# Kernel tuning notes

Hardware: AMD Instinct MI355X
Metric: run time of the kernel (lower is better)

## Reference

```python
import jax, jax.numpy as jnp
import numpy as np

D_MODEL = 2048
K_DIM = 128
V_DIM = 128
H = 16
B = 1
S = 2048
SCALE_BASE = 512.0
THETA = 10000.0
EPS = 1e-5


def setup_inputs() -> dict:
    key = jax.random.key(0)
    ks = jax.random.split(key, 11)
    lin = lambda k, i, o: jax.random.normal(k, (i, o), jnp.float32) * 0.02
    return {
        "x": jax.random.normal(ks[0], (B, S, D_MODEL), jnp.float32),
        "Wq": lin(ks[1], D_MODEL, K_DIM * H), "bq": jnp.zeros((K_DIM * H,), jnp.float32),
        "Wk": lin(ks[2], D_MODEL, K_DIM * H), "bk": jnp.zeros((K_DIM * H,), jnp.float32),
        "Wv": lin(ks[3], D_MODEL, V_DIM * H), "bv": jnp.zeros((V_DIM * H,), jnp.float32),
        "Wg": lin(ks[4], D_MODEL, V_DIM * H), "bg": jnp.zeros((V_DIM * H,), jnp.float32),
        "Wo": lin(ks[5], V_DIM * H, D_MODEL), "bo": jnp.zeros((D_MODEL,), jnp.float32),
    }


def _rotate_half(x):
    # interleaved pairs: (x0, x1, x2, x3, ...) -> (-x1, x0, -x3, x2, ...)
    xr = x.reshape(*x.shape[:-1], -1, 2)
    x1, x2 = xr[..., 0], xr[..., 1]
    return jnp.stack((-x2, x1), axis=-1).reshape(x.shape)


def _rope_xpos(q, k, seq_len, dim):
    pos = jnp.arange(seq_len, dtype=jnp.float32)
    inv_freq = 1.0 / (THETA ** (jnp.arange(0, dim, 2, dtype=jnp.float32) / dim))
    freqs = jnp.repeat(pos[:, None] * inv_freq[None, :], 2, axis=-1)  # (S, dim)
    cos, sin = jnp.cos(freqs), jnp.sin(freqs)
    sbase = (jnp.arange(0, dim, 2, dtype=jnp.float32) + 0.4 * dim) / (1.4 * dim)
    power = (pos - seq_len // 2) / SCALE_BASE
    scale = jnp.repeat(sbase[None, :] ** power[:, None], 2, axis=-1)  # (S, dim)
    q = (q * cos + _rotate_half(q) * sin) * scale
    k = (k * cos + _rotate_half(k) * sin) / scale
    return q, k


def reference(x, Wq, bq, Wk, bk, Wv, bv, Wg, bg, Wo, bo):
    Bb, Ss, Dd = x.shape
    heads = lambda t: t.reshape(Bb, Ss, H, -1).transpose(0, 2, 1, 3)  # (B,H,S,d)
    q = heads(x @ Wq + bq)
    k = heads(x @ Wk + bk)
    v = heads(x @ Wv + bv)
    q, k = _rope_xpos(q, k, Ss, K_DIM)
    # per-head decay gamma_h = 1 - 2^{-5-h}
    gamma = 1.0 - 2.0 ** (-5.0 - jnp.arange(H, dtype=jnp.float32))
    pos = jnp.arange(Ss, dtype=jnp.float32)
    pm = pos[:, None] - pos[None, :]  # (S,S)
    decay_mask = jnp.where(pm >= 0, gamma[:, None, None] ** jnp.maximum(pm, 0.0), 0.0)  # (H,S,S)
    scores = jnp.einsum('bhid,bhjd->bhij', q, k) * decay_mask
    ret = jnp.einsum('bhij,bhjd->bhid', scores, v)  # (B,H,S,V_DIM)
    # concat heads and GroupNorm (num_groups=H, affine=False) over flattened rows
    concat = ret.transpose(0, 2, 1, 3).reshape(Bb * Ss, H, V_DIM)
    mu = concat.mean(-1, keepdims=True)
    var = ((concat - mu) ** 2).mean(-1, keepdims=True)
    gn = ((concat - mu) / jnp.sqrt(var + EPS)).reshape(Bb, Ss, H * V_DIM)
    out = (jax.nn.silu(x @ Wg + bg) * gn) @ Wo + bo
    return out
```

## Files before the change

kernel.cpp:

```cpp
#include <hip/hip_runtime.h>
#include <hip/hip_bf16.h>

#define S 2048
#define DM 2048
#define H 16
#define HD 128

using bf16 = __hip_bfloat16;
typedef __attribute__((ext_vector_type(8))) short bf16x8;
typedef __attribute__((ext_vector_type(8))) unsigned short u16x8;
typedef __attribute__((ext_vector_type(4))) float f32x4;

__device__ __forceinline__ unsigned short f2bu(float f) {
  bf16 b = __float2bfloat16(f);
  union { bf16 b; unsigned short u; } cv; cv.b = b; return cv.u;
}
__device__ __forceinline__ float bu2f(unsigned short u) {
  union { bf16 b; unsigned short u; } cv; cv.u = u; return __bfloat162float(cv.b);
}

__device__ __forceinline__ void async_copy16(const void* g, void* l) {
  __builtin_amdgcn_global_load_lds(
      (const __attribute__((address_space(1))) void*)g,
      (__attribute__((address_space(3))) void*)l, 16, 0, 0);
}

__global__ __launch_bounds__(256) void cvt_kernel(const float* __restrict__ x,
                                                  unsigned short* __restrict__ o) {
  int i = (blockIdx.x * 256 + threadIdx.x) * 4;
  float4 v = *(const float4*)(x + i);
  ushort4 r;
  r.x = f2bu(v.x); r.y = f2bu(v.y); r.z = f2bu(v.z); r.w = f2bu(v.w);
  *(ushort4*)(o + i) = r;
}

__global__ __launch_bounds__(256) void wtrans_kernel(
    const float* __restrict__ s0, const float* __restrict__ s1, const float* __restrict__ s2,
    const float* __restrict__ s3, const float* __restrict__ s4,
    unsigned short* __restrict__ d0, unsigned short* __restrict__ d1, unsigned short* __restrict__ d2,
    unsigned short* __restrict__ d3, unsigned short* __restrict__ d4) {
  __shared__ float tile[64][65];
  int z = blockIdx.z;
  const float* src = z == 0 ? s0 : z == 1 ? s1 : z == 2 ? s2 : z == 3 ? s3 : s4;
  unsigned short* dst = z == 0 ? d0 : z == 1 ? d1 : z == 2 ? d2 : z == 3 ? d3 : d4;
  int tid = threadIdx.x;
  int by = blockIdx.y * 64;
  int bx = blockIdx.x * 64;
  int r0 = tid >> 4;
  int c0 = (tid & 15) * 4;
#pragma unroll
  for (int i = 0; i < 4; i++) {
    int row = r0 + i * 16;
    float4 t = *(const float4*)(src + (size_t)(by + row) * DM + bx + c0);
    tile[row][c0 + 0] = t.x; tile[row][c0 + 1] = t.y;
    tile[row][c0 + 2] = t.z; tile[row][c0 + 3] = t.w;
  }
  __syncthreads();
#pragma unroll
  for (int i = 0; i < 4; i++) {
    int nrow = r0 + i * 16;
    ushort4 o;
    o.x = f2bu(tile[c0 + 0][nrow]);
    o.y = f2bu(tile[c0 + 1][nrow]);
    o.z = f2bu(tile[c0 + 2][nrow]);
    o.w = f2bu(tile[c0 + 3][nrow]);
    *(ushort4*)(dst + (size_t)(bx + nrow) * DM + by + c0) = o;
  }
}

__global__ __launch_bounds__(256) void vtrans_kernel(const unsigned short* __restrict__ v,
                                                     unsigned short* __restrict__ vt) {
  __shared__ unsigned short tile[64][72];
  int tid = threadIdx.x;
  int by = blockIdx.y * 64, bx = blockIdx.x * 64;
  int r0 = tid >> 3;
  int c0 = (tid & 7) * 8;
#pragma unroll
  for (int i = 0; i < 2; i++) {
    int row = r0 + i * 32;
    u16x8 t = *(const u16x8*)(v + (size_t)(by + row) * DM + bx + c0);
#pragma unroll
    for (int j = 0; j < 8; j++) tile[row][c0 + j] = t[j];
  }
  __syncthreads();
#pragma unroll
  for (int i = 0; i < 2; i++) {
    int nrow = r0 + i * 32;
    u16x8 o;
#pragma unroll
    for (int j = 0; j < 8; j++) o[j] = tile[c0 + j][nrow];
    *(u16x8*)(vt + (size_t)(bx + nrow) * DM + by + c0) = o;
  }
}

__device__ __forceinline__ void stage_half(const unsigned short* gbase, char* ldsbase, int tid) {
#pragma unroll
  for (int r = 0; r < 2; r++) {
    int a = r * 8192 + tid * 16;
    int row = a >> 7;
    int cb = (a & 127) ^ ((row & 7) << 4);
    async_copy16((const unsigned char*)(gbase + (size_t)row * DM) + cb, ldsbase + a);
  }
}

__global__ __launch_bounds__(512, 2) void gemm_qkvg_kernel(
    const unsigned short* __restrict__ A, const unsigned short* __restrict__ Bm,
    const float* __restrict__ bias0, const float* __restrict__ bias1,
    const float* __restrict__ bias2, const float* __restrict__ bias3,
    unsigned short* __restrict__ C0, unsigned short* __restrict__ C1,
    unsigned short* __restrict__ C2, unsigned short* __restrict__ C3) {
  __shared__ alignas(16) char smem[131072];
  char* sA = smem;
  char* sB = smem + 65536;
  int tid = threadIdx.x;
  int wg = blockIdx.y * 32 + blockIdx.x;
  int xcd = wg & 7, rr0 = wg >> 3;
  int bm = (rr0 >> 2) * 256;
  int bn = (xcd * 4 + (rr0 & 3)) * 256;
  int wid = tid >> 6, lane = tid & 63;
  int wm = wid >> 2, wn = wid & 3;
  int r16 = lane & 15, quad = lane >> 4;
  f32x4 acc[8][4] = {};
  bf16x8 bfrag[2][4];
  const int bhalf = (wn >> 1) << 14;
  const int blr0 = ((wn & 1) << 6) + r16;

  stage_half(Bm + (size_t)bn * DM, sB, tid);
  stage_half(Bm + (size_t)(bn + 128) * DM, sB + 16384, tid);
  stage_half(A + (size_t)bm * DM, sA, tid);
  stage_half(A + (size_t)(bm + 128) * DM, sA + 16384, tid);
  asm volatile("s_waitcnt vmcnt(0)" ::: "memory");
  __builtin_amdgcn_s_barrier();

  for (int t = 0; t < 32; ++t) {
    const int buf = (t & 1) << 15;
    const int nbuf = buf ^ 32768;
    const bool more = t < 31;
    const int kn = (t + 1) * 64;
    char* sAc = sA + buf;
    char* sBc = sB + buf;
    bf16x8 afrag[4];

#pragma unroll
    for (int nt = 0; nt < 4; ++nt) {
      int lr = blr0 + nt * 16;
      bfrag[0][nt] = *(const bf16x8*)(sBc + bhalf + lr * 128 + ((quad * 16) ^ ((lr & 7) << 4)));
    }
#pragma unroll
    for (int mt = 0; mt < 4; ++mt) {
      int lr = mt * 32 + wm * 16 + r16;
      afrag[mt] = *(const bf16x8*)(sAc + lr * 128 + ((quad * 16) ^ ((lr & 7) << 4)));
    }
    if (more) {
      stage_half(Bm + (size_t)bn * DM + kn, sB + nbuf, tid);
      stage_half(Bm + (size_t)(bn + 128) * DM + kn, sB + nbuf + 16384, tid);
      stage_half(A + (size_t)bm * DM + kn, sA + nbuf, tid);
    }
    __builtin_amdgcn_s_barrier();
    asm volatile("s_waitcnt lgkmcnt(0)" ::: "memory");
    __builtin_amdgcn_s_setprio(1);
#pragma unroll
    for (int mt = 0; mt < 4; ++mt)
#pragma unroll
      for (int nt = 0; nt < 4; ++nt)
        acc[mt][nt] = __builtin_amdgcn_mfma_f32_16x16x32_bf16(afrag[mt], bfrag[0][nt], acc[mt][nt], 0, 0, 0);
    __builtin_amdgcn_s_setprio(0);
    __builtin_amdgcn_s_barrier();

#pragma unroll
    for (int nt = 0; nt < 4; ++nt) {
      int lr = blr0 + nt * 16;
      bfrag[1][nt] = *(const bf16x8*)(sBc + bhalf + lr * 128 + ((64 + quad * 16) ^ ((lr & 7) << 4)));
    }
#pragma unroll
    for (int mt = 0; mt < 4; ++mt) {
      int lr = mt * 32 + wm * 16 + r16;
      afrag[mt] = *(const bf16x8*)(sAc + lr * 128 + ((64 + quad * 16) ^ ((lr & 7) << 4)));
    }
    __builtin_amdgcn_s_barrier();
    asm volatile("s_waitcnt lgkmcnt(0)" ::: "memory");
    __builtin_amdgcn_s_setprio(1);
#pragma unroll
    for (int mt = 0; mt < 4; ++mt)
#pragma unroll
      for (int nt = 0; nt < 4; ++nt)
        acc[mt][nt] = __builtin_amdgcn_mfma_f32_16x16x32_bf16(afrag[mt], bfrag[1][nt], acc[mt][nt], 0, 0, 0);
    __builtin_amdgcn_s_setprio(0);
    if (more) { asm volatile("s_waitcnt vmcnt(6)" ::: "memory"); }
    else      { asm volatile("s_waitcnt vmcnt(0)" ::: "memory"); }
    __builtin_amdgcn_s_barrier();

#pragma unroll
    for (int mt = 0; mt < 4; ++mt) {
      int lr = mt * 32 + wm * 16 + r16;
      afrag[mt] = *(const bf16x8*)(sAc + 16384 + lr * 128 + ((quad * 16) ^ ((lr & 7) << 4)));
    }
    if (more) stage_half(A + (size_t)(bm + 128) * DM + kn, sA + nbuf + 16384, tid);
    __builtin_amdgcn_s_barrier();
    asm volatile("s_waitcnt lgkmcnt(0)" ::: "memory");
    __builtin_amdgcn_s_setprio(1);
#pragma unroll
    for (int mt = 0; mt < 4; ++mt)
#pragma unroll
      for (int nt = 0; nt < 4; ++nt)
        acc[4 + mt][nt] = __builtin_amdgcn_mfma_f32_16x16x32_bf16(afrag[mt], bfrag[0][nt], acc[4 + mt][nt], 0, 0, 0);
    __builtin_amdgcn_s_setprio(0);
    __builtin_amdgcn_s_barrier();

#pragma unroll
    for (int mt = 0; mt < 4; ++mt) {
      int lr = mt * 32 + wm * 16 + r16;
      afrag[mt] = *(const bf16x8*)(sAc + 16384 + lr * 128 + ((64 + quad * 16) ^ ((lr & 7) << 4)));
    }
    __builtin_amdgcn_s_barrier();
    asm volatile("s_waitcnt lgkmcnt(0)" ::: "memory");
    __builtin_amdgcn_s_setprio(1);
#pragma unroll
    for (int mt = 0; mt < 4; ++mt)
#pragma unroll
      for (int nt = 0; nt < 4; ++nt)
        acc[4 + mt][nt] = __builtin_amdgcn_mfma_f32_16x16x32_bf16(afrag[mt], bfrag[1][nt], acc[4 + mt][nt], 0, 0, 0);
    __builtin_amdgcn_s_setprio(0);
    if (more) { asm volatile("s_waitcnt vmcnt(2)" ::: "memory"); }
    __builtin_amdgcn_s_barrier();
  }

  int ch = bn >> 11;
  const float* bp = ch == 0 ? bias0 : ch == 1 ? bias1 : ch == 2 ? bias2 : bias3;
  unsigned short* Cp = ch == 0 ? C0 : ch == 1 ? C1 : ch == 2 ? C2 : C3;
  int lcb = bn & 2047;
#pragma unroll
  for (int nt = 0; nt < 4; ++nt) {
    int lc = lcb + wn * 64 + nt * 16 + r16;
    float bv = bp[lc];
#pragma unroll
    for (int mt = 0; mt < 8; ++mt) {
      int m0 = bm + (mt >> 2) * 128 + (mt & 3) * 32 + wm * 16 + quad * 4;
#pragma unroll
      for (int rrr = 0; rrr < 4; ++rrr)
        Cp[(size_t)(m0 + rrr) * DM + lc] = f2bu(acc[mt][nt][rrr] + bv);
    }
  }
}

__global__ __launch_bounds__(256) void gemm_out_kernel(
    const unsigned short* __restrict__ A, const unsigned short* __restrict__ Bp,
    const float* __restrict__ bias, float* __restrict__ C) {
  __shared__ alignas(16) unsigned char sA[16384];
  __shared__ alignas(16) unsigned char sB[16384];
  int tid = threadIdx.x;
  int bm = blockIdx.y * 128, bn = blockIdx.x * 128;
  int wid = tid >> 6, lane = tid & 63;
  int wm = wid >> 1, wn = wid & 1;
  int r16 = lane & 15, quad = lane >> 4;
  f32x4 acc[4][4] = {};
  for (int kt = 0; kt < DM; kt += 64) {
#pragma unroll
    for (int r = 0; r < 4; r++) {
      int a = r * 4096 + tid * 16;
      int row = a >> 7;
      int cb = (a & 127) ^ ((row & 7) << 4);
      async_copy16((const unsigned char*)(A + (size_t)(bm + row) * DM + kt) + cb, sA + a);
      async_copy16((const unsigned char*)(Bp + (size_t)(bn + row) * DM + kt) + cb, sB + a);
    }
    __syncthreads();
#pragma unroll
    for (int kk = 0; kk < 2; kk++) {
      bf16x8 af[4], bfr[4];
#pragma unroll
      for (int mt = 0; mt < 4; mt++) {
        int row = wm * 64 + mt * 16 + r16;
        af[mt] = *(const bf16x8*)(sA + row * 128 + ((quad * 16 + kk * 64) ^ ((row & 7) << 4)));
      }
#pragma unroll
      for (int nt = 0; nt < 4; nt++) {
        int row = wn * 64 + nt * 16 + r16;
        bfr[nt] = *(const bf16x8*)(sB + row * 128 + ((quad * 16 + kk * 64) ^ ((row & 7) << 4)));
      }
#pragma unroll
      for (int mt = 0; mt < 4; mt++)
#pragma unroll
        for (int nt = 0; nt < 4; nt++)
          acc[mt][nt] = __builtin_amdgcn_mfma_f32_16x16x32_bf16(af[mt], bfr[nt], acc[mt][nt], 0, 0, 0);
    }
    __syncthreads();
  }
#pragma unroll
  for (int nt = 0; nt < 4; nt++) {
    int n = bn + wn * 64 + nt * 16 + r16;
    float bv = bias[n];
#pragma unroll
    for (int mt = 0; mt < 4; mt++) {
      int m0 = bm + wm * 64 + mt * 16 + quad * 4;
#pragma unroll
      for (int r = 0; r < 4; r++)
        C[(size_t)(m0 + r) * DM + n] = acc[mt][nt][r] + bv;
    }
  }
}

__global__ __launch_bounds__(256) void rope_kernel(unsigned short* __restrict__ q,
                                                   unsigned short* __restrict__ k) {
  int idx = blockIdx.x * 256 + threadIdx.x;
  int s = idx >> 10;
  int p = idx & 1023;
  int t = p & 63;
  int head = p >> 6;
  int col = (head << 7) + (t << 1);
  size_t off = (size_t)s * DM + col;
  float ang = (float)s * exp2f((float)(-2 * t) * (13.287712379549449f / 128.0f));
  float sn, cs;
  sincosf(ang, &sn, &cs);
  float sb = ((float)(2 * t) + 51.2f) * (1.0f / 179.2f);
  float power = ((float)s - 1024.0f) * (1.0f / 512.0f);
  float scale = exp2f(power * log2f(sb));
  float l2g = log2f(1.0f - exp2f((float)(-5 - head)));
  float qsc = scale * exp2f((float)s * l2g);
  float ksc = (1.0f / scale) * exp2f(-(float)s * l2g);
  unsigned int qu = *(unsigned int*)(q + off);
  float a = bu2f(qu & 0xffff), b = bu2f(qu >> 16);
  float qa = (a * cs - b * sn) * qsc;
  float qb2 = (b * cs + a * sn) * qsc;
  *(unsigned int*)(q + off) = (unsigned int)f2bu(qa) | ((unsigned int)f2bu(qb2) << 16);
  unsigned int ku = *(unsigned int*)(k + off);
  float c2 = bu2f(ku & 0xffff), d2 = bu2f(ku >> 16);
  float ka = (c2 * cs - d2 * sn) * ksc;
  float kb2 = (d2 * cs + c2 * sn) * ksc;
  *(unsigned int*)(k + off) = (unsigned int)f2bu(ka) | ((unsigned int)f2bu(kb2) << 16);
}

__device__ __forceinline__ void stage_kv(const unsigned short* __restrict__ k,
                                         const unsigned short* __restrict__ vt,
                                         int h, int J0, unsigned char* dK,
                                         unsigned char* dV, int tid) {
#pragma unroll
  for (int r = 0; r < 4; r++) {
    int a = r * 4096 + tid * 16;
    int rowk = a >> 8;
    int cbk = (a & 255) ^ ((rowk & 7) << 4);
    async_copy16((const unsigned char*)(k + (size_t)(J0 + rowk) * DM + h * HD) + cbk, dK + a);
    int rowv = a >> 7;
    int cbv = (a & 127) ^ ((rowv & 7) << 4);
    async_copy16((const unsigned char*)(vt + (size_t)(h * HD + rowv) * DM + J0) + cbv, dV + a);
  }
}

__global__ __launch_bounds__(256) void retention_kernel(
    const unsigned short* __restrict__ q, const unsigned short* __restrict__ k,
    const unsigned short* __restrict__ vt, float* __restrict__ ret) {
  __shared__ alignas(16) unsigned char sK[2][16384];
  __shared__ alignas(16) unsigned char sV[2][16384];
  __shared__ alignas(16) unsigned char Plds[8192];
  int bx = blockIdx.x;
  int hi = bx >> 8;
  int h = ((bx >> 5) & 7) | (hi << 3);
  int ib = hi ? (bx & 31) : (31 - (bx & 31));
  int I = ib << 6;
  int tid = threadIdx.x, wid = tid >> 6, lane = tid & 63;
  int r16 = lane & 15, quad = lane >> 4;
  bf16x8 aQ[4];
  size_t qrow = (size_t)(I + wid * 16 + r16);
#pragma unroll
  for (int kk = 0; kk < 4; kk++)
    aQ[kk] = *(const bf16x8*)(q + qrow * DM + h * HD + kk * 32 + quad * 8);
  f32x4 acc[8] = {};
  unsigned char* Pw = Plds + wid * 2048;
  stage_kv(k, vt, h, 0, sK[0], sV[0], tid);
  for (int J0 = 0; J0 <= I; J0 += 64) {
    int cur = (J0 >> 6) & 1;
    bool more = (J0 + 64) <= I;
    if (more) stage_kv(k, vt, h, J0 + 64, sK[cur ^ 1], sV[cur ^ 1], tid);
    if (more) { asm volatile("s_waitcnt vmcnt(8)" ::: "memory"); }
    else      { asm volatile("s_waitcnt vmcnt(0)" ::: "memory"); }
    __builtin_amdgcn_s_barrier();
    const unsigned char* sKc = sK[cur];
    const unsigned char* sVc = sV[cur];
    f32x4 sf[4] = {};
#pragma unroll
    for (int nt = 0; nt < 4; nt++) {
      int row = nt * 16 + r16;
#pragma unroll
      for (int kk = 0; kk < 4; kk++) {
        bf16x8 bK = *(const bf16x8*)(sKc + row * 256 + ((kk * 64 + quad * 16) ^ ((row & 7) << 4)));
        sf[nt] = __builtin_amdgcn_mfma_f32_16x16x32_bf16(aQ[kk], bK, sf[nt], 0, 0, 0);
      }
    }
    bool diag = (J0 == I);
#pragma unroll
    for (int nt = 0; nt < 4; nt++) {
      int j = nt * 16 + r16;
#pragma unroll
      for (int r = 0; r < 4; r++) {
        int ii = wid * 16 + quad * 4 + r;
        float pv = sf[nt][r];
        if (diag && (ii - j) < 0) pv = 0.0f;
        int pr = quad * 4 + r;
        int pcb = (nt * 16 + r16) * 2;
        *(unsigned short*)(Pw + pr * 128 + (pcb ^ ((pr & 7) << 4))) = f2bu(pv);
      }
    }
#pragma unroll
    for (int kk2 = 0; kk2 < 2; kk2++) {
      int cb = kk2 * 64 + quad * 16;
      bf16x8 aP = *(const bf16x8*)(Pw + r16 * 128 + (cb ^ ((r16 & 7) << 4)));
#pragma unroll
      for (int nt2 = 0; nt2 < 8; nt2++) {
        int row = nt2 * 16 + r16;
        bf16x8 bV = *(const bf16x8*)(sVc + row * 128 + ((kk2 * 64 + quad * 16) ^ ((row & 7) << 4)));
        acc[nt2] = __builtin_amdgcn_mfma_f32_16x16x32_bf16(aP, bV, acc[nt2], 0, 0, 0);
      }
    }
    __builtin_amdgcn_s_barrier();
  }
#pragma unroll
  for (int nt2 = 0; nt2 < 8; nt2++) {
    int dcol = h * HD + nt2 * 16 + r16;
#pragma unroll
    for (int r = 0; r < 4; r++) {
      int i = I + wid * 16 + quad * 4 + r;
      ret[(size_t)i * DM + dcol] = acc[nt2][r];
    }
  }
}

__global__ __launch_bounds__(256) void gn_gate_kernel(const float* __restrict__ ret,
                                                      const unsigned short* __restrict__ g,
                                                      unsigned short* __restrict__ y) {
  int tid = threadIdx.x;
  int wave = tid >> 6, lane = tid & 63;
  int gidx = blockIdx.x * 4 + wave;
  int s = gidx >> 4, h = gidx & 15;
  size_t base = (size_t)s * DM + h * HD + lane * 2;
  float2 v = *(const float2*)(ret + base);
  float sum = v.x + v.y;
  float sq = v.x * v.x + v.y * v.y;
#pragma unroll
  for (int o = 32; o > 0; o >>= 1) {
    sum += __shfl_xor(sum, o, 64);
    sq += __shfl_xor(sq, o, 64);
  }
  float mean = sum * 0.0078125f;
  float var = sq * 0.0078125f - mean * mean;
  float rstd = rsqrtf(var + 1e-5f);
  unsigned int gu = *(const unsigned int*)(g + base);
  float g0 = bu2f(gu & 0xffff), g1 = bu2f(gu >> 16);
  float s0 = g0 / (1.0f + expf(-g0));
  float s1 = g1 / (1.0f + expf(-g1));
  float y0 = s0 * (v.x - mean) * rstd;
  float y1 = s1 * (v.y - mean) * rstd;
  *(unsigned int*)(y + base) = (unsigned int)f2bu(y0) | ((unsigned int)f2bu(y1) << 16);
}

extern "C" void kernel_launch(void* const* d_in, const int* in_sizes, int n_in,
                              void* d_out, int out_size, void* d_ws, size_t ws_size,
                              hipStream_t stream) {
  (void)in_sizes; (void)n_in; (void)out_size; (void)ws_size;
  const float* x  = (const float*)d_in[0];
  const float* Wq = (const float*)d_in[1];
  const float* bq = (const float*)d_in[2];
  const float* Wk = (const float*)d_in[3];
  const float* bk = (const float*)d_in[4];
  const float* Wv = (const float*)d_in[5];
  const float* bv = (const float*)d_in[6];
  const float* Wg = (const float*)d_in[7];
  const float* bg = (const float*)d_in[8];
  const float* Wo = (const float*)d_in[9];
  const float* bo = (const float*)d_in[10];

  char* ws = (char*)d_ws;
  const size_t MB = 1ull << 20;
  unsigned short* xb   = (unsigned short*)(ws + 0 * MB);
  unsigned short* wcat = (unsigned short*)(ws + 8 * MB);
  unsigned short* wto  = (unsigned short*)(ws + 40 * MB);
  unsigned short* qb   = (unsigned short*)(ws + 48 * MB);
  unsigned short* kb   = (unsigned short*)(ws + 56 * MB);
  unsigned short* vb   = (unsigned short*)(ws + 64 * MB);
  unsigned short* gb   = (unsigned short*)(ws + 72 * MB);
  unsigned short* vt   = (unsigned short*)(ws + 80 * MB);
  float*          rt   = (float*)(ws + 88 * MB);
  unsigned short* yb   = (unsigned short*)(ws + 104 * MB);

  cvt_kernel<<<4096, 256, 0, stream>>>(x, xb);
  wtrans_kernel<<<dim3(32, 32, 5), 256, 0, stream>>>(
      Wq, Wk, Wv, Wg, Wo,
      wcat, wcat + (size_t)2048 * DM, wcat + (size_t)4096 * DM, wcat + (size_t)6144 * DM, wto);
  gemm_qkvg_kernel<<<dim3(32, 8), 512, 0, stream>>>(
      xb, wcat, bq, bk, bv, bg, qb, kb, vb, gb);
  rope_kernel<<<8192, 256, 0, stream>>>(qb, kb);
  vtrans_kernel<<<dim3(32, 32), 256, 0, stream>>>(vb, vt);
  retention_kernel<<<512, 256, 0, stream>>>(qb, kb, vt, rt);
  gn_gate_kernel<<<8192, 256, 0, stream>>>(rt, gb, yb);
  gemm_out_kernel<<<dim3(16, 16), 256, 0, stream>>>(yb, wto, bo, (float*)d_out);
}
```

Baseline: 191.6 us.

## Fuse V transpose into QKVG GEMM epilogue and GroupNorm+gate into retention

The QKVG GEMM now writes the V slice directly in transposed layout, which removes the separate vtrans kernel. The retention kernel computes the per-head GroupNorm statistics and the SiLU gate in registers and writes bf16 y. This drops the fp32 ret round trip and the gn_gate launch. The GEMM also changes its workgroup-to-tile swizzle and spreads its async prefetch stages across the four MFMA phases, with the vmcnt waits adjusted to match. The trade-offs are strided transposed stores in the V epilogue and scalar 2-byte gate loads and y stores in the retention epilogue.

```diff
diff --git a/kernel.cpp b/kernel.cpp
--- a/kernel.cpp
+++ b/kernel.cpp
@@ -68,31 +68,6 @@
   }
 }
 
-__global__ __launch_bounds__(256) void vtrans_kernel(const unsigned short* __restrict__ v,
-                                                     unsigned short* __restrict__ vt) {
-  __shared__ unsigned short tile[64][72];
-  int tid = threadIdx.x;
-  int by = blockIdx.y * 64, bx = blockIdx.x * 64;
-  int r0 = tid >> 3;
-  int c0 = (tid & 7) * 8;
-#pragma unroll
-  for (int i = 0; i < 2; i++) {
-    int row = r0 + i * 32;
-    u16x8 t = *(const u16x8*)(v + (size_t)(by + row) * DM + bx + c0);
-#pragma unroll
-    for (int j = 0; j < 8; j++) tile[row][c0 + j] = t[j];
-  }
-  __syncthreads();
-#pragma unroll
-  for (int i = 0; i < 2; i++) {
-    int nrow = r0 + i * 32;
-    u16x8 o;
-#pragma unroll
-    for (int j = 0; j < 8; j++) o[j] = tile[c0 + j][nrow];
-    *(u16x8*)(vt + (size_t)(bx + nrow) * DM + by + c0) = o;
-  }
-}
-
 __device__ __forceinline__ void stage_half(const unsigned short* gbase, char* ldsbase, int tid) {
 #pragma unroll
   for (int r = 0; r < 2; r++) {
@@ -108,15 +83,15 @@
     const float* __restrict__ bias0, const float* __restrict__ bias1,
     const float* __restrict__ bias2, const float* __restrict__ bias3,
     unsigned short* __restrict__ C0, unsigned short* __restrict__ C1,
-    unsigned short* __restrict__ C2, unsigned short* __restrict__ C3) {
+    unsigned short* __restrict__ Vt, unsigned short* __restrict__ C3) {
   __shared__ alignas(16) char smem[131072];
   char* sA = smem;
   char* sB = smem + 65536;
   int tid = threadIdx.x;
   int wg = blockIdx.y * 32 + blockIdx.x;
-  int xcd = wg & 7, rr0 = wg >> 3;
-  int bm = (rr0 >> 2) * 256;
-  int bn = (xcd * 4 + (rr0 & 3)) * 256;
+  int swz = (wg & 7) * 32 + (wg >> 3);
+  int bm = (swz >> 5) * 256;
+  int bn = (swz & 31) * 256;
   int wid = tid >> 6, lane = tid & 63;
   int wm = wid >> 2, wn = wid & 3;
   int r16 = lane & 15, quad = lane >> 4;
@@ -151,11 +126,7 @@
       int lr = mt * 32 + wm * 16 + r16;
       afrag[mt] = *(const bf16x8*)(sAc + lr * 128 + ((quad * 16) ^ ((lr & 7) << 4)));
     }
-    if (more) {
-      stage_half(Bm + (size_t)bn * DM + kn, sB + nbuf, tid);
-      stage_half(Bm + (size_t)(bn + 128) * DM + kn, sB + nbuf + 16384, tid);
-      stage_half(A + (size_t)bm * DM + kn, sA + nbuf, tid);
-    }
+    if (more) stage_half(Bm + (size_t)bn * DM + kn, sB + nbuf, tid);
     __builtin_amdgcn_s_barrier();
     asm volatile("s_waitcnt lgkmcnt(0)" ::: "memory");
     __builtin_amdgcn_s_setprio(1);
@@ -177,6 +148,7 @@
       int lr = mt * 32 + wm * 16 + r16;
       afrag[mt] = *(const bf16x8*)(sAc + lr * 128 + ((64 + quad * 16) ^ ((lr & 7) << 4)));
     }
+    if (more) stage_half(Bm + (size_t)(bn + 128) * DM + kn, sB + nbuf + 16384, tid);
     __builtin_amdgcn_s_barrier();
     asm volatile("s_waitcnt lgkmcnt(0)" ::: "memory");
     __builtin_amdgcn_s_setprio(1);
@@ -186,7 +158,7 @@
       for (int nt = 0; nt < 4; ++nt)
         acc[mt][nt] = __builtin_amdgcn_mfma_f32_16x16x32_bf16(afrag[mt], bfrag[1][nt], acc[mt][nt], 0, 0, 0);
     __builtin_amdgcn_s_setprio(0);
-    if (more) { asm volatile("s_waitcnt vmcnt(6)" ::: "memory"); }
+    if (more) { asm volatile("s_waitcnt vmcnt(4)" ::: "memory"); }
     else      { asm volatile("s_waitcnt vmcnt(0)" ::: "memory"); }
     __builtin_amdgcn_s_barrier();
 
@@ -195,7 +167,7 @@
       int lr = mt * 32 + wm * 16 + r16;
       afrag[mt] = *(const bf16x8*)(sAc + 16384 + lr * 128 + ((quad * 16) ^ ((lr & 7) << 4)));
     }
-    if (more) stage_half(A + (size_t)(bm + 128) * DM + kn, sA + nbuf + 16384, tid);
+    if (more) stage_half(A + (size_t)bm * DM + kn, sA + nbuf, tid);
     __builtin_amdgcn_s_barrier();
     asm volatile("s_waitcnt lgkmcnt(0)" ::: "memory");
     __builtin_amdgcn_s_setprio(1);
@@ -212,6 +184,7 @@
       int lr = mt * 32 + wm * 16 + r16;
       afrag[mt] = *(const bf16x8*)(sAc + 16384 + lr * 128 + ((64 + quad * 16) ^ ((lr & 7) << 4)));
     }
+    if (more) stage_half(A + (size_t)(bm + 128) * DM + kn, sA + nbuf + 16384, tid);
     __builtin_amdgcn_s_barrier();
     asm volatile("s_waitcnt lgkmcnt(0)" ::: "memory");
     __builtin_amdgcn_s_setprio(1);
@@ -227,18 +200,36 @@
 
   int ch = bn >> 11;
   const float* bp = ch == 0 ? bias0 : ch == 1 ? bias1 : ch == 2 ? bias2 : bias3;
-  unsigned short* Cp = ch == 0 ? C0 : ch == 1 ? C1 : ch == 2 ? C2 : C3;
   int lcb = bn & 2047;
-#pragma unroll
-  for (int nt = 0; nt < 4; ++nt) {
-    int lc = lcb + wn * 64 + nt * 16 + r16;
-    float bv = bp[lc];
-#pragma unroll
-    for (int mt = 0; mt < 8; ++mt) {
-      int m0 = bm + (mt >> 2) * 128 + (mt & 3) * 32 + wm * 16 + quad * 4;
-#pragma unroll
-      for (int rrr = 0; rrr < 4; ++rrr)
-        Cp[(size_t)(m0 + rrr) * DM + lc] = f2bu(acc[mt][nt][rrr] + bv);
+  if (ch == 2) {
+#pragma unroll
+    for (int nt = 0; nt < 4; ++nt) {
+      int lc = lcb + wn * 64 + nt * 16 + r16;
+      float bv = bp[lc];
+#pragma unroll
+      for (int mt = 0; mt < 8; ++mt) {
+        int m0 = bm + (mt >> 2) * 128 + (mt & 3) * 32 + wm * 16 + quad * 4;
+        ushort4 o;
+        o.x = f2bu(acc[mt][nt][0] + bv);
+        o.y = f2bu(acc[mt][nt][1] + bv);
+        o.z = f2bu(acc[mt][nt][2] + bv);
+        o.w = f2bu(acc[mt][nt][3] + bv);
+        *(ushort4*)(Vt + (size_t)lc * DM + m0) = o;
+      }
+    }
+  } else {
+    unsigned short* Cp = ch == 0 ? C0 : ch == 1 ? C1 : C3;
+#pragma unroll
+    for (int nt = 0; nt < 4; ++nt) {
+      int lc = lcb + wn * 64 + nt * 16 + r16;
+      float bv = bp[lc];
+#pragma unroll
+      for (int mt = 0; mt < 8; ++mt) {
+        int m0 = bm + (mt >> 2) * 128 + (mt & 3) * 32 + wm * 16 + quad * 4;
+#pragma unroll
+        for (int rr = 0; rr < 4; ++rr)
+          Cp[(size_t)(m0 + rr) * DM + lc] = f2bu(acc[mt][nt][rr] + bv);
+      }
     }
   }
 }
@@ -347,7 +338,8 @@
 
 __global__ __launch_bounds__(256) void retention_kernel(
     const unsigned short* __restrict__ q, const unsigned short* __restrict__ k,
-    const unsigned short* __restrict__ vt, float* __restrict__ ret) {
+    const unsigned short* __restrict__ vt, const unsigned short* __restrict__ g,
+    unsigned short* __restrict__ y) {
   __shared__ alignas(16) unsigned char sK[2][16384];
   __shared__ alignas(16) unsigned char sV[2][16384];
   __shared__ alignas(16) unsigned char Plds[8192];
@@ -413,42 +405,32 @@
     __builtin_amdgcn_s_barrier();
   }
 #pragma unroll
-  for (int nt2 = 0; nt2 < 8; nt2++) {
-    int dcol = h * HD + nt2 * 16 + r16;
-#pragma unroll
-    for (int r = 0; r < 4; r++) {
-      int i = I + wid * 16 + quad * 4 + r;
-      ret[(size_t)i * DM + dcol] = acc[nt2][r];
-    }
-  }
-}
-
-__global__ __launch_bounds__(256) void gn_gate_kernel(const float* __restrict__ ret,
-                                                      const unsigned short* __restrict__ g,
-                                                      unsigned short* __restrict__ y) {
-  int tid = threadIdx.x;
-  int wave = tid >> 6, lane = tid & 63;
-  int gidx = blockIdx.x * 4 + wave;
-  int s = gidx >> 4, h = gidx & 15;
-  size_t base = (size_t)s * DM + h * HD + lane * 2;
-  float2 v = *(const float2*)(ret + base);
-  float sum = v.x + v.y;
-  float sq = v.x * v.x + v.y * v.y;
-#pragma unroll
-  for (int o = 32; o > 0; o >>= 1) {
-    sum += __shfl_xor(sum, o, 64);
-    sq += __shfl_xor(sq, o, 64);
-  }
-  float mean = sum * 0.0078125f;
-  float var = sq * 0.0078125f - mean * mean;
-  float rstd = rsqrtf(var + 1e-5f);
-  unsigned int gu = *(const unsigned int*)(g + base);
-  float g0 = bu2f(gu & 0xffff), g1 = bu2f(gu >> 16);
-  float s0 = g0 / (1.0f + expf(-g0));
-  float s1 = g1 / (1.0f + expf(-g1));
-  float y0 = s0 * (v.x - mean) * rstd;
-  float y1 = s1 * (v.y - mean) * rstd;
-  *(unsigned int*)(y + base) = (unsigned int)f2bu(y0) | ((unsigned int)f2bu(y1) << 16);
+  for (int r = 0; r < 4; r++) {
+    float sum = 0.0f, sq = 0.0f;
+#pragma unroll
+    for (int nt2 = 0; nt2 < 8; nt2++) {
+      float v = acc[nt2][r];
+      sum += v; sq += v * v;
+    }
+#pragma unroll
+    for (int o = 1; o <= 8; o <<= 1) {
+      sum += __shfl_xor(sum, o, 64);
+      sq += __shfl_xor(sq, o, 64);
+    }
+    float mean = sum * 0.0078125f;
+    float var = sq * 0.0078125f - mean * mean;
+    float rstd = rsqrtf(var + 1e-5f);
+    int i = I + wid * 16 + quad * 4 + r;
+    size_t rowbase = (size_t)i * DM + h * HD;
+#pragma unroll
+    for (int nt2 = 0; nt2 < 8; nt2++) {
+      int col = nt2 * 16 + r16;
+      float gv = bu2f(g[rowbase + col]);
+      float sg = gv / (1.0f + expf(-gv));
+      float yv = sg * (acc[nt2][r] - mean) * rstd;
+      y[rowbase + col] = f2bu(yv);
+    }
+  }
 }
 
 extern "C" void kernel_launch(void* const* d_in, const int* in_sizes, int n_in,
@@ -474,10 +456,8 @@
   unsigned short* wto  = (unsigned short*)(ws + 40 * MB);
   unsigned short* qb   = (unsigned short*)(ws + 48 * MB);
   unsigned short* kb   = (unsigned short*)(ws + 56 * MB);
-  unsigned short* vb   = (unsigned short*)(ws + 64 * MB);
   unsigned short* gb   = (unsigned short*)(ws + 72 * MB);
   unsigned short* vt   = (unsigned short*)(ws + 80 * MB);
-  float*          rt   = (float*)(ws + 88 * MB);
   unsigned short* yb   = (unsigned short*)(ws + 104 * MB);
 
   cvt_kernel<<<4096, 256, 0, stream>>>(x, xb);
@@ -485,10 +465,8 @@
       Wq, Wk, Wv, Wg, Wo,
       wcat, wcat + (size_t)2048 * DM, wcat + (size_t)4096 * DM, wcat + (size_t)6144 * DM, wto);
   gemm_qkvg_kernel<<<dim3(32, 8), 512, 0, stream>>>(
-      xb, wcat, bq, bk, bv, bg, qb, kb, vb, gb);
+      xb, wcat, bq, bk, bv, bg, qb, kb, vt, gb);
   rope_kernel<<<8192, 256, 0, stream>>>(qb, kb);
-  vtrans_kernel<<<dim3(32, 32), 256, 0, stream>>>(vb, vt);
-  retention_kernel<<<512, 256, 0, stream>>>(qb, kb, vt, rt);
-  gn_gate_kernel<<<8192, 256, 0, stream>>>(rt, gb, yb);
+  retention_kernel<<<512, 256, 0, stream>>>(qb, kb, vt, gb, yb);
   gemm_out_kernel<<<dim3(16, 16), 256, 0, stream>>>(yb, wto, bo, (float*)d_out);
 }
```

Result: faster. 182.3 us (-4.8%).
